# Performance work log

Measured on AMD Instinct MI355X. Metric: run time of the kernel, lower is better.

## Reference

```python
import jax, jax.numpy as jnp
import numpy as np

EMBED_DIM = 768
NUM_HEADS = 12
EPS = 1e-6


def setup_inputs() -> dict:
    key = jax.random.key(0)
    ks = jax.random.split(key, 9)
    B, C, H, W = 8, EMBED_DIM, 48, 48
    std = 0.02
    E = EMBED_DIM
    return {
        "query": jax.random.normal(ks[0], (B, C, H, W), dtype=jnp.float32),
        "Wq": jax.random.normal(ks[1], (E, E), dtype=jnp.float32) * std,
        "bq": jnp.zeros((E,), dtype=jnp.float32),
        "Wk": jax.random.normal(ks[2], (E, E), dtype=jnp.float32) * std,
        "bk": jnp.zeros((E,), dtype=jnp.float32),
        "Wv": jax.random.normal(ks[3], (E, E), dtype=jnp.float32) * std,
        "bv": jnp.zeros((E,), dtype=jnp.float32),
        "Wo": jax.random.normal(ks[4], (E, E), dtype=jnp.float32) * std,
        "bo": jnp.zeros((E,), dtype=jnp.float32),
    }


def reference(query, Wq, bq, Wk, bk, Wv, bv, Wo, bo):
    # query: (B, C, H, W) -> (L, B, E) with L = H*W
    B, C, H, W = query.shape
    L = H * W
    E = C
    h = NUM_HEADS
    d = E // h
    x = query.reshape(B, C, L).transpose(2, 0, 1)  # (L, B, E)

    # cos/sin positional reweighting: pi/2 * (i+1) / L
    idx = (jnp.pi / 2) * jnp.arange(1, L + 1, dtype=x.dtype) / L
    sin = jnp.sin(idx)[None, :, None]  # (1, L, 1)
    cos = jnp.cos(idx)[None, :, None]

    # projections + relu feature map
    q = jax.nn.relu(x @ Wq.T + bq)
    k = jax.nn.relu(x @ Wk.T + bk)
    v = x @ Wv.T + bv

    def to_heads(t):  # (L, B, E) -> (B*h, L, d)
        return t.reshape(L, B * h, d).transpose(1, 0, 2)

    q, k, v = to_heads(q), to_heads(k), to_heads(v)

    q_ = jnp.concatenate([q * sin, q * cos], axis=-1)  # (n, L, 2d)
    k_ = jnp.concatenate([k * sin, k * cos], axis=-1)

    # non-causal linear attention
    kv = jnp.einsum("nld,nlm->ndm", k_, v)              # (n, 2d, d)
    z = 1.0 / jnp.maximum(jnp.einsum("nld,nd->nl", q_, k_.sum(axis=1)), EPS)
    out = jnp.einsum("nld,ndm,nl->nlm", q_, kv, z)       # (n, L, d)

    # residual (DropPath is identity at inference)
    attn = x + out.transpose(1, 0, 2).reshape(L, B, E)
    return attn @ Wo.T + bo
```

## Files before the change

### kernel.cpp

```cpp
#include <hip/hip_runtime.h>


#define L_SEQ 2304
#define BATCH 8
#define EDIM 768
#define NHEAD 12
#define DHEAD 64
#define MROWS (L_SEQ * BATCH)

typedef __attribute__((ext_vector_type(8))) short bf16x8_t;
typedef __attribute__((ext_vector_type(4))) float f32x4_t;

__device__ __forceinline__ float b2f(unsigned short u) {
  union { unsigned int i; float f; } x; x.i = ((unsigned int)u) << 16; return x.f;
}
__device__ __forceinline__ unsigned short f2b(float f) {
  union { float f; unsigned int i; } x; x.f = f;
  unsigned int r = x.i + 0x7FFFu + ((x.i >> 16) & 1u);
  return (unsigned short)(r >> 16);
}

#define GLOAD_LDS16(g, l)                                                     \
  __builtin_amdgcn_global_load_lds(                                           \
      (const __attribute__((address_space(1))) unsigned int*)(g),             \
      (__attribute__((address_space(3))) unsigned int*)(l), 16, 0, 0)

__global__ __launch_bounds__(256) void conv_w(
    const float* __restrict__ W0, const float* __restrict__ W1,
    const float* __restrict__ W2, const float* __restrict__ W3,
    unsigned short* __restrict__ dst) {
  const float* W = (blockIdx.y == 0) ? W0 : (blockIdx.y == 1) ? W1
                 : (blockIdx.y == 2) ? W2 : W3;
  unsigned short* d = dst + (size_t)blockIdx.y * EDIM * EDIM;
  int idx = blockIdx.x * 256 + threadIdx.x;
  float4 v = *(const float4*)(W + (size_t)idx * 4);
  ushort4 o;
  o.x = f2b(v.x); o.y = f2b(v.y); o.z = f2b(v.z); o.w = f2b(v.w);
  *(ushort4*)(d + (size_t)idx * 4) = o;
}

__global__ __launch_bounds__(256) void transpose_q(
    const float* __restrict__ q, unsigned short* __restrict__ xT) {
  __shared__ float tile[64][65];
  int b = blockIdx.z;
  int e0 = blockIdx.x * 64;
  int l0 = blockIdx.y * 64;
  int t = threadIdx.x;
  int li = t & 63, er = t >> 6;
#pragma unroll
  for (int p = 0; p < 16; p++) {
    int eo = er + p * 4;
    tile[eo][li] = q[((size_t)b * EDIM + (e0 + eo)) * L_SEQ + (l0 + li)];
  }
  __syncthreads();
  int ei = t & 63, lr = t >> 6;
#pragma unroll
  for (int p = 0; p < 16; p++) {
    int lo = lr + p * 4;
    xT[((size_t)b * L_SEQ + (l0 + lo)) * EDIM + (e0 + ei)] = f2b(tile[ei][lo]);
  }
}

#define ALDSO(b_, h_) ((b_) * 16384 + (h_) * 8192)
#define BLDSO(b_, h_) (32768 + (b_) * 16384 + (h_) * 8192)

#define BAR() __builtin_amdgcn_s_barrier()
#define LGKM0() asm volatile("s_waitcnt lgkmcnt(0)")
#define LGKM8() asm volatile("s_waitcnt lgkmcnt(8)")
#define VMW(N) asm volatile("s_waitcnt vmcnt(" #N ")" ::: "memory")

#define STG_A(h_, kt_, LB_)                                                          \
  {                                                                                  \
    GLOAD_LDS16(a_sb + (size_t)((h_) * 128) * EDIM + (kt_) * 64, lds + (LB_) + t * 8); \
    GLOAD_LDS16(a_sb + (size_t)((h_) * 128 + 64) * EDIM + (kt_) * 64,                \
                lds + (LB_) + 4096 + t * 8);                                         \
  }
#define STG_B(h_, kt_, LB_)                                                          \
  {                                                                                  \
    GLOAD_LDS16(b_sb + (size_t)((h_) * 128) * EDIM + (kt_) * 64, lds + (LB_) + t * 8); \
    GLOAD_LDS16(b_sb + (size_t)((h_) * 128 + 64) * EDIM + (kt_) * 64,                \
                lds + (LB_) + 4096 + t * 8);                                         \
  }

#define DS_A(SET, B_, H_)                                                            \
  _Pragma("unroll") for (int i_ = 0; i_ < 4; i_++)                                   \
  _Pragma("unroll") for (int kk_ = 0; kk_ < 2; kk_++)                                \
    SET[i_][kk_] = *(const bf16x8_t*)(lds + ALDSO(B_, H_) +                          \
                                      ((a_base + i_ * 1024 + kk_ * 32) ^ xorv));

#define DS_B(SET, B_, H_)                                                            \
  _Pragma("unroll") for (int j_ = 0; j_ < 2; j_++)                                   \
  _Pragma("unroll") for (int kk_ = 0; kk_ < 2; kk_++)                                \
    SET[j_][kk_] = *(const bf16x8_t*)(lds + BLDSO(B_, H_) +                          \
                                      ((b_base + j_ * 1024 + kk_ * 32) ^ xorv));

#define MFMAQ(ASET, BSET, AH, BH)                                                    \
  __builtin_amdgcn_s_setprio(1);                                                     \
  _Pragma("unroll") for (int i_ = 0; i_ < 4; i_++)                                   \
  _Pragma("unroll") for (int j_ = 0; j_ < 2; j_++)                                   \
  _Pragma("unroll") for (int kk_ = 0; kk_ < 2; kk_++)                                \
    acc[(AH) * 4 + i_][(BH) * 2 + j_] = __builtin_amdgcn_mfma_f32_16x16x32_bf16(     \
        ASET[i_][kk_], BSET[j_][kk_], acc[(AH) * 4 + i_][(BH) * 2 + j_], 0, 0, 0);   \
  __builtin_amdgcn_s_setprio(0);

template <int MODE>
__global__ __launch_bounds__(512, 2) void gemm256(
    const unsigned short* __restrict__ A,
    const unsigned short* __restrict__ Wall,
    const float* __restrict__ bias0, const float* __restrict__ bias1,
    const float* __restrict__ bias2,
    unsigned short* __restrict__ dst0, unsigned short* __restrict__ dst1,
    unsigned short* __restrict__ dst2,
    float* __restrict__ dstf) {
  extern __shared__ __align__(16) unsigned short lds[];

  const unsigned short* W;
  const float* bias;
  unsigned short* dst = nullptr;
  bool do_relu = false;
  int rowblk, colblk;
  {
    int nwg = (int)gridDim.x;
    int wg = ((int)blockIdx.x & 7) * (nwg >> 3) + ((int)blockIdx.x >> 3);
    if (MODE == 0) {
      rowblk = wg / 9;
      int c = wg - rowblk * 9;
      colblk = c % 3;
      int z = c / 3;
      W = Wall + (size_t)z * EDIM * EDIM;
      bias = (z == 0) ? bias0 : (z == 1) ? bias1 : bias2;
      dst = (z == 0) ? dst0 : (z == 1) ? dst1 : dst2;
      do_relu = (z < 2);
    } else {
      rowblk = wg / 3;
      colblk = wg - rowblk * 3;
      W = Wall;
      bias = bias0;
    }
  }
  const int row0 = rowblk * 256;
  const int col0 = colblk * 256;

  const int t = threadIdx.x;
  const int lane = t & 63;
  const int wave = t >> 6;
  const int wm = wave >> 2;
  const int wn = wave & 3;
  const int mrow = lane & 15;
  const int quad = lane >> 4;

  const int xorv = (mrow & 7) << 3;
  const int a_base = (wm * 64 + mrow) * 64 + quad * 8;
  const int b_base = (wn * 32 + mrow) * 64 + quad * 8;

  const int lr_s = t >> 3;
  const int k0_s = ((((t >> 3) & 7) ^ (t & 7)) << 3);
  const unsigned short* a_sb = A + (size_t)(row0 + lr_s) * EDIM + k0_s;
  const unsigned short* b_sb = W + (size_t)(col0 + lr_s) * EDIM + k0_s;

  f32x4_t acc[8][4] = {};
  bf16x8_t aA[4][2], aB[4][2], bA[2][2], bB[2][2];

  STG_A(0, 0, ALDSO(0, 0));
  STG_B(0, 0, BLDSO(0, 0));
  STG_A(1, 0, ALDSO(0, 1));
  STG_B(1, 0, BLDSO(0, 1));
  STG_A(0, 1, ALDSO(1, 0));
  STG_B(0, 1, BLDSO(1, 0));
  VMW(4);
  BAR();

#pragma unroll
  for (int i = 0; i < 6; ++i) {
    const int kt0 = 2 * i, kt1 = 2 * i + 1;
    const bool nxt = (i < 5);
    DS_A(aA, 0, 0);
    DS_B(bA, 0, 0);
    STG_A(1, kt1, ALDSO(1, 1));
    LGKM8();
    BAR();
    MFMAQ(aA, bA, 0, 0);
    LGKM0();
    BAR();
    DS_B(bB, 0, 1);
    STG_B(1, kt1, BLDSO(1, 1));
    BAR();
    MFMAQ(aA, bB, 0, 1);
    LGKM0();
    BAR();
    DS_A(aB, 0, 1);
    if (nxt) STG_A(0, kt0 + 2, ALDSO(0, 0));
    BAR();
    MFMAQ(aB, bA, 1, 0);
    LGKM0();
    BAR();
    if (nxt) STG_B(0, kt0 + 2, BLDSO(0, 0));
    BAR();
    MFMAQ(aB, bB, 1, 1);
    if (nxt) { VMW(4); } else { VMW(0); }
    BAR();
    DS_A(aA, 1, 0);
    DS_B(bA, 1, 0);
    if (nxt) STG_A(1, kt0 + 2, ALDSO(0, 1));
    LGKM8();
    BAR();
    MFMAQ(aA, bA, 0, 0);
    LGKM0();
    BAR();
    DS_B(bB, 1, 1);
    if (nxt) STG_B(1, kt0 + 2, BLDSO(0, 1));
    BAR();
    MFMAQ(aA, bB, 0, 1);
    LGKM0();
    BAR();
    DS_A(aB, 1, 1);
    if (nxt) STG_A(0, kt1 + 2, ALDSO(1, 0));
    BAR();
    MFMAQ(aB, bA, 1, 0);
    LGKM0();
    BAR();
    if (nxt) STG_B(0, kt1 + 2, BLDSO(1, 0));
    BAR();
    MFMAQ(aB, bB, 1, 1);
    if (nxt) { VMW(4); } else { VMW(0); }
    BAR();
  }

  const int bb = row0 / L_SEQ;
#pragma unroll
  for (int ti = 0; ti < 8; ti++) {
    int rbase = row0 + (ti >> 2) * 128 + wm * 64 + (ti & 3) * 16 + quad * 4;
#pragma unroll
    for (int tj = 0; tj < 4; tj++) {
      int gc = col0 + (tj >> 1) * 128 + wn * 32 + (tj & 1) * 16 + mrow;
      float bv = bias[gc];
#pragma unroll
      for (int r = 0; r < 4; r++) {
        int gr = rbase + r;
        float v = acc[ti][tj][r] + bv;
        if (MODE == 0) {
          if (do_relu) v = fmaxf(v, 0.0f);
          int ll = gr - bb * L_SEQ;
          int n = bb * NHEAD + (gc >> 6);
          dst[((size_t)n * L_SEQ + ll) * DHEAD + (gc & 63)] = f2b(v);
        } else {
          dstf[(size_t)gr * EDIM + gc] = v;
        }
      }
    }
  }
}

__global__ __launch_bounds__(256) void kv_mfma(
    const unsigned short* __restrict__ kbuf, const unsigned short* __restrict__ vbuf,
    float* __restrict__ kv, float* __restrict__ ksum) {
  constexpr int ST = 40;
  __shared__ __align__(16) unsigned short ksT[128 * ST];
  __shared__ __align__(16) unsigned short vsT[80 * ST];
  int n = blockIdx.x;
  int lbase = blockIdx.y * 288;
  int t = threadIdx.x;
  int lane = t & 63, wave = t >> 6;
  int mrow = lane & 15, quad = lane >> 4;

  for (int i = t; i < 16 * ST; i += 256) {
    int row = i / ST, col = i % ST;
    vsT[(64 + row) * ST + col] = (row == 0 && col < 32) ? (unsigned short)0x3F80 : 0;
  }

  int lrd = t >> 3;
  int oct = t & 7;
  const unsigned short* kbase = kbuf + (size_t)n * L_SEQ * DHEAD + oct * 8;
  const unsigned short* vbase = vbuf + (size_t)n * L_SEQ * DHEAD + oct * 8;

  f32x4_t acc[2][5] = {};

  for (int s = 0; s < 9; s++) {
    int l = lbase + s * 32 + lrd;
    float sv, cv;
    sincosf(1.5707963267948966f * (float)(l + 1) / 2304.0f, &sv, &cv);
    union { uint4 q; unsigned short u[8]; } kq, vq;
    kq.q = *(const uint4*)(kbase + (size_t)l * DHEAD);
    vq.q = *(const uint4*)(vbase + (size_t)l * DHEAD);
    __syncthreads();
#pragma unroll
    for (int e = 0; e < 8; e++) {
      int d = oct * 8 + e;
      float kval = b2f(kq.u[e]);
      ksT[d * ST + lrd] = f2b(kval * sv);
      ksT[(64 + d) * ST + lrd] = f2b(kval * cv);
      vsT[d * ST + lrd] = vq.u[e];
    }
    __syncthreads();
    bf16x8_t af[2];
#pragma unroll
    for (int ti = 0; ti < 2; ti++)
      af[ti] = *(const bf16x8_t*)(ksT + ((wave * 2 + ti) * 16 + mrow) * ST + quad * 8);
#pragma unroll
    for (int tj = 0; tj < 5; tj++) {
      bf16x8_t bfv = *(const bf16x8_t*)(vsT + (tj * 16 + mrow) * ST + quad * 8);
#pragma unroll
      for (int ti = 0; ti < 2; ti++)
        acc[ti][tj] = __builtin_amdgcn_mfma_f32_16x16x32_bf16(af[ti], bfv, acc[ti][tj], 0, 0, 0);
    }
  }

#pragma unroll
  for (int ti = 0; ti < 2; ti++) {
#pragma unroll
    for (int r = 0; r < 4; r++) {
      int j = (wave * 2 + ti) * 16 + quad * 4 + r;
#pragma unroll
      for (int tj = 0; tj < 4; tj++) {
        int m = tj * 16 + mrow;
        atomicAdd(&kv[((size_t)n * 128 + j) * 64 + m], acc[ti][tj][r]);
      }
      if (mrow == 0) atomicAdd(&ksum[n * 128 + j], acc[ti][4][r]);
    }
  }
}

__global__ __launch_bounds__(256) void attn_mfma(
    const unsigned short* __restrict__ qbuf, const float* __restrict__ kv,
    const float* __restrict__ ksum, const unsigned short* __restrict__ xT,
    unsigned short* __restrict__ attn) {
  __shared__ __align__(16) unsigned short As[128 * 72];
  __shared__ __align__(16) unsigned short Bs[64 * 136];
  __shared__ float ks_l[128];
  __shared__ float zs[128], zc[128];
  int l0 = blockIdx.x * 128;
  int n = blockIdx.y;
  int t = threadIdx.x;
  int lane = t & 63, wave = t >> 6;
  int mrow = lane & 15, quad = lane >> 4;
  int b = n / NHEAD, hd = n % NHEAD;

  {
    int row = t >> 1, off = (t & 1) * 32;
    const unsigned short* src = qbuf + ((size_t)n * L_SEQ + l0 + row) * DHEAD + off;
    unsigned short* d = As + row * 72 + off;
#pragma unroll
    for (int c = 0; c < 4; c++)
      *(uint4*)(d + c * 8) = *(const uint4*)(src + c * 8);
  }
  {
    int j = t >> 1, mh = (t & 1) * 32;
    const float* src = kv + ((size_t)n * 128 + j) * 64 + mh;
#pragma unroll
    for (int mm = 0; mm < 32; mm++)
      Bs[(mh + mm) * 136 + j] = f2b(src[mm]);
  }
  if (t < 128) ks_l[t] = ksum[n * 128 + t];
  __syncthreads();

  if (t < 128) {
    float d0 = 0.f, d1 = 0.f;
    const unsigned short* arow = As + t * 72;
#pragma unroll
    for (int j = 0; j < 8; j++) {
      bf16x8_t v = *(const bf16x8_t*)(arow + j * 8);
#pragma unroll
      for (int e = 0; e < 8; e++) {
        float qv = b2f((unsigned short)v[e]);
        d0 += qv * ks_l[j * 8 + e];
        d1 += qv * ks_l[64 + j * 8 + e];
      }
    }
    float sv, cv;
    sincosf(1.5707963267948966f * (float)(l0 + t + 1) / 2304.0f, &sv, &cv);
    float z = 1.0f / fmaxf(sv * d0 + cv * d1, 1e-6f);
    zs[t] = z * sv;
    zc[t] = z * cv;
  }
  __syncthreads();

  int wr = wave * 32;
  f32x4_t acc0[2][4] = {}, acc1[2][4] = {};
#pragma unroll
  for (int ks = 0; ks < 2; ks++) {
    bf16x8_t af[2];
#pragma unroll
    for (int ti = 0; ti < 2; ti++)
      af[ti] = *(const bf16x8_t*)(As + (wr + ti * 16 + mrow) * 72 + ks * 32 + quad * 8);
#pragma unroll
    for (int tj = 0; tj < 4; tj++) {
      bf16x8_t b0 = *(const bf16x8_t*)(Bs + (tj * 16 + mrow) * 136 + ks * 32 + quad * 8);
      bf16x8_t b1 = *(const bf16x8_t*)(Bs + (tj * 16 + mrow) * 136 + 64 + ks * 32 + quad * 8);
#pragma unroll
      for (int ti = 0; ti < 2; ti++) {
        acc0[ti][tj] = __builtin_amdgcn_mfma_f32_16x16x32_bf16(af[ti], b0, acc0[ti][tj], 0, 0, 0);
        acc1[ti][tj] = __builtin_amdgcn_mfma_f32_16x16x32_bf16(af[ti], b1, acc1[ti][tj], 0, 0, 0);
      }
    }
  }

#pragma unroll
  for (int ti = 0; ti < 2; ti++) {
#pragma unroll
    for (int tj = 0; tj < 4; tj++) {
      int m = tj * 16 + mrow;
#pragma unroll
      for (int r = 0; r < 4; r++) {
        int row = wr + ti * 16 + quad * 4 + r;
        int l = l0 + row;
        float ov = zs[row] * acc0[ti][tj][r] + zc[row] * acc1[ti][tj][r];
        float xv = b2f(xT[((size_t)b * L_SEQ + l) * EDIM + hd * DHEAD + m]);
        attn[((size_t)l * BATCH + b) * EDIM + hd * DHEAD + m] = f2b(xv + ov);
      }
    }
  }
}

extern "C" void kernel_launch(void* const* d_in, const int* in_sizes, int n_in,
                              void* d_out, int out_size, void* d_ws, size_t ws_size,
                              hipStream_t stream) {
  const float* query = (const float*)d_in[0];
  const float* Wq = (const float*)d_in[1];
  const float* bq = (const float*)d_in[2];
  const float* Wk = (const float*)d_in[3];
  const float* bk = (const float*)d_in[4];
  const float* Wv = (const float*)d_in[5];
  const float* bv = (const float*)d_in[6];
  const float* Wo = (const float*)d_in[7];
  const float* bo = (const float*)d_in[8];
  float* out = (float*)d_out;

  unsigned short* xT = (unsigned short*)d_out;

  char* ws = (char*)d_ws;
  const size_t SZ = (size_t)MROWS * EDIM * 2;
  unsigned short* qbuf = (unsigned short*)(ws);
  unsigned short* kbuf = (unsigned short*)(ws + SZ);
  unsigned short* vbuf = (unsigned short*)(ws + 2 * SZ);
  unsigned short* attn = kbuf;
  float* kv   = (float*)(ws + 3 * SZ);
  float* ksum = (float*)(ws + 3 * SZ + 3145728);
  unsigned short* wbf = (unsigned short*)(ws + 3 * SZ + 3145728 + 49152);

  static bool attr_done = false;
  if (!attr_done) {
    (void)hipFuncSetAttribute((const void*)gemm256<0>,
                              hipFuncAttributeMaxDynamicSharedMemorySize, 131072);
    (void)hipFuncSetAttribute((const void*)gemm256<1>,
                              hipFuncAttributeMaxDynamicSharedMemorySize, 131072);
    attr_done = true;
  }

  conv_w<<<dim3(576, 4), 256, 0, stream>>>(Wq, Wk, Wv, Wo, wbf);

  transpose_q<<<dim3(12, 36, 8), 256, 0, stream>>>(query, xT);

  gemm256<0><<<dim3(648), dim3(512), 131072, stream>>>(
      xT, wbf, bq, bk, bv, qbuf, kbuf, vbuf, nullptr);

  hipMemsetAsync(ws + 3 * SZ, 0, 3145728 + 49152, stream);

  kv_mfma<<<dim3(96, 8), 256, 0, stream>>>(kbuf, vbuf, kv, ksum);

  attn_mfma<<<dim3(L_SEQ / 128, 96), 256, 0, stream>>>(qbuf, kv, ksum, xT, attn);

  gemm256<1><<<dim3(216), dim3(512), 131072, stream>>>(
      attn, wbf + 3 * (size_t)EDIM * EDIM, bo, nullptr, nullptr,
      nullptr, nullptr, nullptr, out);
}
```

Measured before the change: 297.3 us.

## Merge prep kernels and memset, store kv transposed, compute ksum on VALU

Fuses the weight bf16 conversion, the input transpose and the zeroing of the kv/ksum accumulators into one prep launch, which removes two launches and a memset. kv_mfma now takes V as the A operand and K features as B, producing kv transposed, and drops the ones-row MFMA trick for ksum in favour of per-thread sums reduced through LDS atomics. attn_mfma then reads kvT contiguously with float4 loads instead of doing strided scalar loads. The cost is more VALU work and shared-memory atomics in kv_mfma, plus a more complex prep kernel.

```diff
diff --git a/kernel.cpp b/kernel.cpp
--- a/kernel.cpp
+++ b/kernel.cpp
@@ -25,39 +25,45 @@
       (const __attribute__((address_space(1))) unsigned int*)(g),             \
       (__attribute__((address_space(3))) unsigned int*)(l), 16, 0, 0)
 
-__global__ __launch_bounds__(256) void conv_w(
+__global__ __launch_bounds__(256) void prep(
+    const float* __restrict__ q,
     const float* __restrict__ W0, const float* __restrict__ W1,
     const float* __restrict__ W2, const float* __restrict__ W3,
-    unsigned short* __restrict__ dst) {
-  const float* W = (blockIdx.y == 0) ? W0 : (blockIdx.y == 1) ? W1
-                 : (blockIdx.y == 2) ? W2 : W3;
-  unsigned short* d = dst + (size_t)blockIdx.y * EDIM * EDIM;
-  int idx = blockIdx.x * 256 + threadIdx.x;
-  float4 v = *(const float4*)(W + (size_t)idx * 4);
-  ushort4 o;
-  o.x = f2b(v.x); o.y = f2b(v.y); o.z = f2b(v.z); o.w = f2b(v.w);
-  *(ushort4*)(d + (size_t)idx * 4) = o;
-}
-
-__global__ __launch_bounds__(256) void transpose_q(
-    const float* __restrict__ q, unsigned short* __restrict__ xT) {
+    unsigned short* __restrict__ wbf, unsigned short* __restrict__ xT,
+    float* __restrict__ kvz) {
   __shared__ float tile[64][65];
-  int b = blockIdx.z;
-  int e0 = blockIdx.x * 64;
-  int l0 = blockIdx.y * 64;
+  int bx = blockIdx.x;
   int t = threadIdx.x;
-  int li = t & 63, er = t >> 6;
-#pragma unroll
-  for (int p = 0; p < 16; p++) {
-    int eo = er + p * 4;
-    tile[eo][li] = q[((size_t)b * EDIM + (e0 + eo)) * L_SEQ + (l0 + li)];
-  }
-  __syncthreads();
-  int ei = t & 63, lr = t >> 6;
-#pragma unroll
-  for (int p = 0; p < 16; p++) {
-    int lo = lr + p * 4;
-    xT[((size_t)b * L_SEQ + (l0 + lo)) * EDIM + (e0 + ei)] = f2b(tile[ei][lo]);
+  if (bx < 2304) {
+    int y = bx / 576;
+    const float* W = (y == 0) ? W0 : (y == 1) ? W1 : (y == 2) ? W2 : W3;
+    unsigned short* d = wbf + (size_t)y * EDIM * EDIM;
+    int idx = (bx - y * 576) * 256 + t;
+    float4 v = *(const float4*)(W + (size_t)idx * 4);
+    ushort4 o;
+    o.x = f2b(v.x); o.y = f2b(v.y); o.z = f2b(v.z); o.w = f2b(v.w);
+    *(ushort4*)(d + (size_t)idx * 4) = o;
+  } else if (bx < 5760) {
+    int bb = bx - 2304;
+    int e0 = (bb % 12) * 64;
+    int l0 = ((bb / 12) % 36) * 64;
+    int b = bb / 432;
+    int li = t & 63, er = t >> 6;
+#pragma unroll
+    for (int p = 0; p < 16; p++) {
+      int eo = er + p * 4;
+      tile[eo][li] = q[((size_t)b * EDIM + (e0 + eo)) * L_SEQ + (l0 + li)];
+    }
+    __syncthreads();
+    int ei = t & 63, lr = t >> 6;
+#pragma unroll
+    for (int p = 0; p < 16; p++) {
+      int lo = lr + p * 4;
+      xT[((size_t)b * L_SEQ + (l0 + lo)) * EDIM + (e0 + ei)] = f2b(tile[ei][lo]);
+    }
+  } else {
+    int idx = (bx - 5760) * 256 + t;
+    *(float4*)(kvz + (size_t)idx * 4) = make_float4(0.f, 0.f, 0.f, 0.f);
   }
 }
 
@@ -253,27 +259,26 @@
 
 __global__ __launch_bounds__(256) void kv_mfma(
     const unsigned short* __restrict__ kbuf, const unsigned short* __restrict__ vbuf,
-    float* __restrict__ kv, float* __restrict__ ksum) {
+    float* __restrict__ kvT, float* __restrict__ ksum) {
   constexpr int ST = 40;
   __shared__ __align__(16) unsigned short ksT[128 * ST];
-  __shared__ __align__(16) unsigned short vsT[80 * ST];
+  __shared__ __align__(16) unsigned short vsT[64 * ST];
+  __shared__ float ksum_l[128];
   int n = blockIdx.x;
   int lbase = blockIdx.y * 288;
   int t = threadIdx.x;
   int lane = t & 63, wave = t >> 6;
   int mrow = lane & 15, quad = lane >> 4;
 
-  for (int i = t; i < 16 * ST; i += 256) {
-    int row = i / ST, col = i % ST;
-    vsT[(64 + row) * ST + col] = (row == 0 && col < 32) ? (unsigned short)0x3F80 : 0;
-  }
+  if (t < 128) ksum_l[t] = 0.f;
 
   int lrd = t >> 3;
   int oct = t & 7;
   const unsigned short* kbase = kbuf + (size_t)n * L_SEQ * DHEAD + oct * 8;
   const unsigned short* vbase = vbuf + (size_t)n * L_SEQ * DHEAD + oct * 8;
 
-  f32x4_t acc[2][5] = {};
+  f32x4_t acc[8] = {};
+  float sks[8] = {}, skc[8] = {};
 
   for (int s = 0; s < 9; s++) {
     int l = lbase + s * 32 + lrd;
@@ -287,41 +292,43 @@
     for (int e = 0; e < 8; e++) {
       int d = oct * 8 + e;
       float kval = b2f(kq.u[e]);
-      ksT[d * ST + lrd] = f2b(kval * sv);
-      ksT[(64 + d) * ST + lrd] = f2b(kval * cv);
+      float a = kval * sv, c = kval * cv;
+      ksT[d * ST + lrd] = f2b(a);
+      ksT[(64 + d) * ST + lrd] = f2b(c);
       vsT[d * ST + lrd] = vq.u[e];
+      sks[e] += a;
+      skc[e] += c;
     }
     __syncthreads();
-    bf16x8_t af[2];
-#pragma unroll
-    for (int ti = 0; ti < 2; ti++)
-      af[ti] = *(const bf16x8_t*)(ksT + ((wave * 2 + ti) * 16 + mrow) * ST + quad * 8);
-#pragma unroll
-    for (int tj = 0; tj < 5; tj++) {
-      bf16x8_t bfv = *(const bf16x8_t*)(vsT + (tj * 16 + mrow) * ST + quad * 8);
-#pragma unroll
-      for (int ti = 0; ti < 2; ti++)
-        acc[ti][tj] = __builtin_amdgcn_mfma_f32_16x16x32_bf16(af[ti], bfv, acc[ti][tj], 0, 0, 0);
-    }
-  }
-
-#pragma unroll
-  for (int ti = 0; ti < 2; ti++) {
+    bf16x8_t af = *(const bf16x8_t*)(vsT + (wave * 16 + mrow) * ST + quad * 8);
+#pragma unroll
+    for (int jt = 0; jt < 8; jt++) {
+      bf16x8_t bfk = *(const bf16x8_t*)(ksT + (jt * 16 + mrow) * ST + quad * 8);
+      acc[jt] = __builtin_amdgcn_mfma_f32_16x16x32_bf16(af, bfk, acc[jt], 0, 0, 0);
+    }
+  }
+
+#pragma unroll
+  for (int e = 0; e < 8; e++) {
+    atomicAdd(&ksum_l[oct * 8 + e], sks[e]);
+    atomicAdd(&ksum_l[64 + oct * 8 + e], skc[e]);
+  }
+  __syncthreads();
+  if (t < 128) atomicAdd(&ksum[n * 128 + t], ksum_l[t]);
+
+#pragma unroll
+  for (int jt = 0; jt < 8; jt++) {
 #pragma unroll
     for (int r = 0; r < 4; r++) {
-      int j = (wave * 2 + ti) * 16 + quad * 4 + r;
-#pragma unroll
-      for (int tj = 0; tj < 4; tj++) {
-        int m = tj * 16 + mrow;
-        atomicAdd(&kv[((size_t)n * 128 + j) * 64 + m], acc[ti][tj][r]);
-      }
-      if (mrow == 0) atomicAdd(&ksum[n * 128 + j], acc[ti][4][r]);
+      int m = wave * 16 + quad * 4 + r;
+      int j = jt * 16 + mrow;
+      atomicAdd(&kvT[((size_t)n * 64 + m) * 128 + j], acc[jt][r]);
     }
   }
 }
 
 __global__ __launch_bounds__(256) void attn_mfma(
-    const unsigned short* __restrict__ qbuf, const float* __restrict__ kv,
+    const unsigned short* __restrict__ qbuf, const float* __restrict__ kvT,
     const float* __restrict__ ksum, const unsigned short* __restrict__ xT,
     unsigned short* __restrict__ attn) {
   __shared__ __align__(16) unsigned short As[128 * 72];
@@ -344,11 +351,19 @@
       *(uint4*)(d + c * 8) = *(const uint4*)(src + c * 8);
   }
   {
-    int j = t >> 1, mh = (t & 1) * 32;
-    const float* src = kv + ((size_t)n * 128 + j) * 64 + mh;
-#pragma unroll
-    for (int mm = 0; mm < 32; mm++)
-      Bs[(mh + mm) * 136 + j] = f2b(src[mm]);
+    int m = t >> 2, part = t & 3;
+    const float* src = kvT + ((size_t)n * 64 + m) * 128 + part * 32;
+    unsigned short* dBs = Bs + m * 136 + part * 32;
+#pragma unroll
+    for (int c = 0; c < 4; c++) {
+      float4 a = *(const float4*)(src + c * 8);
+      float4 bq = *(const float4*)(src + c * 8 + 4);
+      ushort4 o1, o2;
+      o1.x = f2b(a.x); o1.y = f2b(a.y); o1.z = f2b(a.z); o1.w = f2b(a.w);
+      o2.x = f2b(bq.x); o2.y = f2b(bq.y); o2.z = f2b(bq.z); o2.w = f2b(bq.w);
+      *(ushort4*)(dBs + c * 8) = o1;
+      *(ushort4*)(dBs + c * 8 + 4) = o2;
+    }
   }
   if (t < 128) ks_l[t] = ksum[n * 128 + t];
   __syncthreads();
@@ -433,7 +448,7 @@
   unsigned short* kbuf = (unsigned short*)(ws + SZ);
   unsigned short* vbuf = (unsigned short*)(ws + 2 * SZ);
   unsigned short* attn = kbuf;
-  float* kv   = (float*)(ws + 3 * SZ);
+  float* kvT  = (float*)(ws + 3 * SZ);
   float* ksum = (float*)(ws + 3 * SZ + 3145728);
   unsigned short* wbf = (unsigned short*)(ws + 3 * SZ + 3145728 + 49152);
 
@@ -446,18 +461,14 @@
     attr_done = true;
   }
 
-  conv_w<<<dim3(576, 4), 256, 0, stream>>>(Wq, Wk, Wv, Wo, wbf);
-
-  transpose_q<<<dim3(12, 36, 8), 256, 0, stream>>>(query, xT);
+  prep<<<dim3(6540), 256, 0, stream>>>(query, Wq, Wk, Wv, Wo, wbf, xT, kvT);
 
   gemm256<0><<<dim3(648), dim3(512), 131072, stream>>>(
       xT, wbf, bq, bk, bv, qbuf, kbuf, vbuf, nullptr);
 
-  hipMemsetAsync(ws + 3 * SZ, 0, 3145728 + 49152, stream);
-
-  kv_mfma<<<dim3(96, 8), 256, 0, stream>>>(kbuf, vbuf, kv, ksum);
-
-  attn_mfma<<<dim3(L_SEQ / 128, 96), 256, 0, stream>>>(qbuf, kv, ksum, xT, attn);
+  kv_mfma<<<dim3(96, 8), 256, 0, stream>>>(kbuf, vbuf, kvT, ksum);
+
+  attn_mfma<<<dim3(L_SEQ / 128, 96), 256, 0, stream>>>(qbuf, kvT, ksum, xT, attn);
 
   gemm256<1><<<dim3(216), dim3(512), 131072, stream>>>(
       attn, wbf + 3 * (size_t)EDIM * EDIM, bo, nullptr, nullptr,
```

After: 300.7 us. About the same (+1.2%).
